# Performance work log

Measured on AMD Instinct MI355X. Metric: run time of the kernel, lower is better.

## Reference

```python
import jax, jax.numpy as jnp
import numpy as np


def _prelu(x, a):
    return jnp.where(x >= 0, x, a * x)


def _conv1x1(x, w, b, a):
    # x: (B,C,H,W), w: (O,C), b: (O,), a: PReLU scalar (shared, torch default)
    y = jnp.einsum('bchw,oc->bohw', x, w) + b[None, :, None, None]
    return _prelu(y, a)


def setup_inputs() -> dict:
    key = jax.random.key(0)
    ks = jax.random.split(key, 7)
    B, C, H, W = 8, 128, 256, 256
    std = 1.0 / np.sqrt(C)
    x = jax.random.normal(ks[0], (B, C, H, W), dtype=jnp.float32)
    Wf = jax.random.normal(ks[1], (C, C), dtype=jnp.float32) * std
    bf = jax.random.normal(ks[2], (C,), dtype=jnp.float32) * std
    Wg = jax.random.normal(ks[3], (C, C), dtype=jnp.float32) * std
    bg = jax.random.normal(ks[4], (C,), dtype=jnp.float32) * std
    Wh = jax.random.normal(ks[5], (C, C), dtype=jnp.float32) * std
    bh = jax.random.normal(ks[6], (C,), dtype=jnp.float32) * std
    af = jnp.float32(0.25)
    ag = jnp.float32(0.25)
    ah = jnp.float32(0.25)
    return {"x": x, "Wf": Wf, "bf": bf, "af": af,
            "Wg": Wg, "bg": bg, "ag": ag,
            "Wh": Wh, "bh": bh, "ah": ah}


def reference(x, Wf, bf, af, Wg, bg, ag, Wh, bh, ah):
    # 1x1 conv projections + PReLU
    map_f = _conv1x1(x, Wf, bf, af)          # (B,C,H,W)
    map_g = _conv1x1(x, Wg, bg, ag)          # (B,C,H,W)
    map_h = _conv1x1(x, Wh, bh, ah)          # (B,C,H,W)
    # map_f.transpose(2,3) @ map_g -> (B,C,W,W), unscaled single-head attention
    atten = jnp.einsum('bchw,bchv->bcwv', map_f, map_g)  # (B,C,W,W)
    atten = jax.nn.softmax(atten, axis=-1)
    # map_h @ atten -> (B,C,H,W)
    out = jnp.einsum('bchw,bcwv->bchv', map_h, atten)
    return out + x
```

## Files before the change

### kernel.cpp

```cpp
#include <hip/hip_runtime.h>

typedef __bf16 bf16_t;
typedef __bf16 bf16x8 __attribute__((ext_vector_type(8)));
typedef __bf16 bf16x4 __attribute__((ext_vector_type(4)));
typedef float  f32x4  __attribute__((ext_vector_type(4)));

#define HW_ 65536
#define C_  128

__device__ __forceinline__ int swz(int r) { return ((r ^ (r >> 3)) & 7) << 4; }

#define LGKM0() asm volatile("s_waitcnt lgkmcnt(0)" ::: "memory")
__device__ __forceinline__ void BAR() {
  asm volatile("" ::: "memory");
  __builtin_amdgcn_s_barrier();
  asm volatile("" ::: "memory");
}

template<bool HBLK>
__device__ __forceinline__ void conv_one(char* lds, const float* __restrict__ Wsrc,
                                         const float* __restrict__ bias, float alpha,
                                         bf16_t* __restrict__ dst, size_t pb,
                                         int wv, int lr, int lq, int t, int s0)
{
  __syncthreads();
  #pragma unroll
  for (int rep = 0; rep < 16; ++rep) {
    int q = rep * 256 + t;
    int o = q >> 5, c0 = (q & 31) * 4;
    f32x4 w4 = *(const f32x4*)(Wsrc + o * C_ + c0);
    bf16x4 v;
    v[0] = (bf16_t)w4[0]; v[1] = (bf16_t)w4[1]; v[2] = (bf16_t)w4[2]; v[3] = (bf16_t)w4[3];
    *(bf16x4*)(lds + 32768 + ((o * 256 + c0 * 2) ^ swz(o))) = v;
  }
  __syncthreads();

  const f32x4 fz = {0.f, 0.f, 0.f, 0.f};
  f32x4 acc[2][8];
  #pragma unroll
  for (int mf = 0; mf < 2; ++mf)
    #pragma unroll
    for (int nf = 0; nf < 8; ++nf)
      acc[mf][nf] = fz;

  #pragma unroll
  for (int ks = 0; ks < 4; ++ks) {
    int kb = ks * 32 + lq * 8;
    bf16x8 a[2], bb[8];
    #pragma unroll
    for (int mf = 0; mf < 2; ++mf) {
      int m = wv * 32 + mf * 16 + lr;
      a[mf] = *(const bf16x8*)(lds + 32768 + ((m * 256 + kb * 2) ^ swz(m)));
    }
    #pragma unroll
    for (int nf = 0; nf < 8; ++nf) {
      int n = nf * 16 + lr;
      bb[nf] = *(const bf16x8*)(lds + ((n * 256 + kb * 2) ^ swz(n)));
    }
    #pragma unroll
    for (int mf = 0; mf < 2; ++mf)
      #pragma unroll
      for (int nf = 0; nf < 8; ++nf)
        acc[mf][nf] = __builtin_amdgcn_mfma_f32_16x16x32_bf16(a[mf], bb[nf], acc[mf][nf], 0, 0, 0);
  }

  #pragma unroll
  for (int mf = 0; mf < 2; ++mf) {
    #pragma unroll
    for (int i = 0; i < 4; ++i) {
      int o = wv * 32 + mf * 16 + lq * 4 + i;
      float bo = bias[o];
      #pragma unroll
      for (int nf = 0; nf < 8; ++nf) {
        int s = s0 + nf * 16 + lr;
        float v = acc[mf][nf][i] + bo;
        v = (v >= 0.f) ? v : alpha * v;
        size_t off;
        if (HBLK) {
          int h = s >> 8, w = s & 255;
          off = pb + (size_t)o * HW_ + (size_t)(w >> 6) * 16384 + h * 64 + (w & 63);
        } else {
          off = pb + (size_t)o * HW_ + s;
        }
        dst[off] = (bf16_t)v;
      }
    }
  }
}

__global__ __launch_bounds__(256, 2) void conv_kernel(
    const float* __restrict__ x,
    const float* __restrict__ Wf, const float* __restrict__ bfp, const float* __restrict__ afp,
    const float* __restrict__ Wg, const float* __restrict__ bgp, const float* __restrict__ agp,
    const float* __restrict__ Wh, const float* __restrict__ bhp, const float* __restrict__ ahp,
    bf16_t* __restrict__ mF, bf16_t* __restrict__ mG, bf16_t* __restrict__ mH, int b0)
{
  __shared__ __align__(16) char lds[65536];
  const int t = threadIdx.x;
  const int bloc = blockIdx.y;
  const int s0 = blockIdx.x * 128;
  const size_t xbase = ((size_t)(b0 + bloc) * C_) * HW_ + s0;

  #pragma unroll
  for (int rep = 0; rep < 4; ++rep) {
    int q = rep * 256 + t;
    int c0 = (q >> 5) * 4, sl0 = (q & 31) * 4;
    f32x4 r[4];
    #pragma unroll
    for (int i = 0; i < 4; ++i)
      r[i] = *(const f32x4*)(x + xbase + (size_t)(c0 + i) * HW_ + sl0);
    #pragma unroll
    for (int js = 0; js < 4; ++js) {
      int s = sl0 + js;
      bf16x4 v;
      v[0] = (bf16_t)r[0][js]; v[1] = (bf16_t)r[1][js];
      v[2] = (bf16_t)r[2][js]; v[3] = (bf16_t)r[3][js];
      *(bf16x4*)(lds + ((s * 256 + c0 * 2) ^ swz(s))) = v;
    }
  }

  const int wv = t >> 6, lane = t & 63, lr = lane & 15, lq = lane >> 4;
  const size_t pb = (size_t)bloc * C_ * HW_;
  conv_one<false>(lds, Wf, bfp, afp[0], mF, pb, wv, lr, lq, t, s0);
  conv_one<false>(lds, Wg, bgp, agp[0], mG, pb, wv, lr, lq, t, s0);
  conv_one<true >(lds, Wh, bhp, ahp[0], mH, pb, wv, lr, lq, t, s0);
}

#define GT_OFF  32768
#define HS_OFF  131072
#define SMAX_OFF 151552
#define SSUM_OFF 153600
#define SMEM_BYTES 155648

__global__ __launch_bounds__(512, 2) void attn_kernel(
    const bf16_t* __restrict__ mF, const bf16_t* __restrict__ mG, const bf16_t* __restrict__ mH,
    const float* __restrict__ x, float* __restrict__ out, int b0)
{
  extern __shared__ __align__(16) char smem[];
  const int t = threadIdx.x;
  const int c = blockIdx.x, bloc = blockIdx.y;
  const int wv = t >> 6, lane = t & 63, lr = lane & 15, lq = lane >> 4;
  const int wr = wv >> 1, wc = wv & 1;
  const size_t plane  = ((size_t)bloc * C_ + c) * HW_;
  const size_t gplane = (((size_t)(b0 + bloc)) * C_ + c) * HW_;

  const f32x4 fz = {0.f, 0.f, 0.f, 0.f};
  f32x4 acc[4][8];
  #pragma unroll
  for (int mf = 0; mf < 4; ++mf)
    #pragma unroll
    for (int nf = 0; nf < 8; ++nf)
      acc[mf][nf] = fz;

  const int hq = t >> 5, wb8 = t & 31;

  bf16x8 pfF[4], pfG[4];
  #pragma unroll
  for (int i = 0; i < 4; ++i) {
    pfF[i] = *(const bf16x8*)(mF + plane + (size_t)(hq * 4 + i) * 256 + wb8 * 8);
    pfG[i] = *(const bf16x8*)(mG + plane + (size_t)(hq * 4 + i) * 256 + wb8 * 8);
  }

  for (int hb = 0; hb < 256; hb += 64) {
    BAR();
    #pragma unroll
    for (int j = 0; j < 8; ++j) {
      int w = wb8 * 8 + j;
      bf16x4 v; v[0] = pfF[0][j]; v[1] = pfF[1][j]; v[2] = pfF[2][j]; v[3] = pfF[3][j];
      *(bf16x4*)(smem + ((w * 128 + hq * 8) ^ swz(w))) = v;
      bf16x4 g; g[0] = pfG[0][j]; g[1] = pfG[1][j]; g[2] = pfG[2][j]; g[3] = pfG[3][j];
      *(bf16x4*)(smem + GT_OFF + ((w * 128 + hq * 8) ^ swz(w))) = g;
    }
    if (hb < 192) {
      #pragma unroll
      for (int i = 0; i < 4; ++i) {
        pfF[i] = *(const bf16x8*)(mF + plane + (size_t)(hb + 64 + hq * 4 + i) * 256 + wb8 * 8);
        pfG[i] = *(const bf16x8*)(mG + plane + (size_t)(hb + 64 + hq * 4 + i) * 256 + wb8 * 8);
      }
    }
    LGKM0(); BAR();
    #pragma unroll
    for (int k0 = 0; k0 < 64; k0 += 32) {
      int kb = k0 + lq * 8;
      bf16x8 a[4], bb[8];
      #pragma unroll
      for (int mf = 0; mf < 4; ++mf) {
        int m = wr * 64 + mf * 16 + lr;
        a[mf] = *(const bf16x8*)(smem + ((m * 128 + kb * 2) ^ swz(m)));
      }
      #pragma unroll
      for (int nf = 0; nf < 8; ++nf) {
        int n = wc * 128 + nf * 16 + lr;
        bb[nf] = *(const bf16x8*)(smem + GT_OFF + ((n * 128 + kb * 2) ^ swz(n)));
      }
      #pragma unroll
      for (int mf = 0; mf < 4; ++mf)
        #pragma unroll
        for (int nf = 0; nf < 8; ++nf)
          acc[mf][nf] = __builtin_amdgcn_mfma_f32_16x16x32_bf16(a[mf], bb[nf], acc[mf][nf], 0, 0, 0);
    }
  }

  float* smax = (float*)(smem + SMAX_OFF);
  float* ssum = (float*)(smem + SSUM_OFF);
  float rowm[4][4];
  #pragma unroll
  for (int mf = 0; mf < 4; ++mf)
    #pragma unroll
    for (int i = 0; i < 4; ++i) {
      float m = acc[mf][0][i];
      #pragma unroll
      for (int nf = 1; nf < 8; ++nf) m = fmaxf(m, acc[mf][nf][i]);
      #pragma unroll
      for (int d = 1; d < 16; d <<= 1) m = fmaxf(m, __shfl_xor(m, d));
      rowm[mf][i] = m;
    }
  if (lr == 0) {
    #pragma unroll
    for (int mf = 0; mf < 4; ++mf)
      #pragma unroll
      for (int i = 0; i < 4; ++i)
        smax[wc * 256 + wr * 64 + mf * 16 + lq * 4 + i] = rowm[mf][i];
  }
  __syncthreads();
  float m2[4][4], rs[4][4];
  #pragma unroll
  for (int mf = 0; mf < 4; ++mf)
    #pragma unroll
    for (int i = 0; i < 4; ++i) {
      int w = wr * 64 + mf * 16 + lq * 4 + i;
      m2[mf][i] = fmaxf(smax[w], smax[256 + w]);
      rs[mf][i] = 0.f;
    }
  #pragma unroll
  for (int mf = 0; mf < 4; ++mf)
    #pragma unroll
    for (int nf = 0; nf < 8; ++nf)
      #pragma unroll
      for (int i = 0; i < 4; ++i) {
        float e = __expf(acc[mf][nf][i] - m2[mf][i]);
        acc[mf][nf][i] = e;
        rs[mf][i] += e;
      }
  #pragma unroll
  for (int mf = 0; mf < 4; ++mf)
    #pragma unroll
    for (int i = 0; i < 4; ++i) {
      float s = rs[mf][i];
      #pragma unroll
      for (int d = 1; d < 16; d <<= 1) s += __shfl_xor(s, d);
      rs[mf][i] = s;
    }
  if (lr == 0) {
    #pragma unroll
    for (int mf = 0; mf < 4; ++mf)
      #pragma unroll
      for (int i = 0; i < 4; ++i)
        ssum[wc * 256 + wr * 64 + mf * 16 + lq * 4 + i] = rs[mf][i];
  }
  __syncthreads();
  #pragma unroll
  for (int mf = 0; mf < 4; ++mf)
    #pragma unroll
    for (int i = 0; i < 4; ++i) {
      int w = wr * 64 + mf * 16 + lq * 4 + i;
      float rinv = 1.f / (ssum[w] + ssum[256 + w]);
      #pragma unroll
      for (int nf = 0; nf < 8; ++nf) {
        int v_ = wc * 128 + nf * 16 + lr;
        *(bf16_t*)(smem + ((v_ * 512 + w * 2) ^ swz(v_))) = (bf16_t)(acc[mf][nf][i] * rinv);
      }
    }

  #pragma unroll
  for (int mf = 0; mf < 4; ++mf)
    #pragma unroll
    for (int nf = 0; nf < 8; ++nf)
      acc[mf][nf] = fz;

  bf16x8 hreg[2];
  {
    const size_t hbase0 = plane;
    #pragma unroll
    for (int rep = 0; rep < 2; ++rep) {
      int u = rep * 512 + t;
      int h = u >> 2, wl0 = (u & 3) * 8;
      hreg[rep] = *(const bf16x8*)(mH + hbase0 + h * 64 + wl0);
    }
  }

  for (int wk = 0; wk < 8; ++wk) {
    LGKM0(); BAR();
    {
      #pragma unroll
      for (int rep = 0; rep < 2; ++rep) {
        int u = rep * 512 + t;
        int h = u >> 2, wl0 = (u & 3) * 8;
        *(bf16x8*)(smem + HS_OFF + h * 80 + wl0 * 2) = hreg[rep];
      }
    }
    if (wk < 7) {
      const size_t hbase = plane + (size_t)((wk + 1) >> 1) * 16384 + (size_t)((wk + 1) & 1) * 32;
      #pragma unroll
      for (int rep = 0; rep < 2; ++rep) {
        int u = rep * 512 + t;
        int h = u >> 2, wl0 = (u & 3) * 8;
        hreg[rep] = *(const bf16x8*)(mH + hbase + h * 64 + wl0);
      }
    }
    LGKM0(); BAR();
    int kb = lq * 8;
    bf16x8 a[4], bb[8];
    #pragma unroll
    for (int mf = 0; mf < 4; ++mf) {
      int m = wr * 64 + mf * 16 + lr;
      a[mf] = *(const bf16x8*)(smem + HS_OFF + m * 80 + kb * 2);
    }
    #pragma unroll
    for (int nf = 0; nf < 8; ++nf) {
      int n = wc * 128 + nf * 16 + lr;
      int kg = wk * 32 + kb;
      bb[nf] = *(const bf16x8*)(smem + ((n * 512 + kg * 2) ^ swz(n)));
    }
    #pragma unroll
    for (int mf = 0; mf < 4; ++mf)
      #pragma unroll
      for (int nf = 0; nf < 8; ++nf)
        acc[mf][nf] = __builtin_amdgcn_mfma_f32_16x16x32_bf16(a[mf], bb[nf], acc[mf][nf], 0, 0, 0);
  }

  #pragma unroll
  for (int mf = 0; mf < 4; ++mf)
    #pragma unroll
    for (int i = 0; i < 4; ++i) {
      int h = wr * 64 + mf * 16 + lq * 4 + i;
      #pragma unroll
      for (int nf = 0; nf < 8; ++nf) {
        int v_ = wc * 128 + nf * 16 + lr;
        size_t off = gplane + (size_t)h * 256 + v_;
        out[off] = acc[mf][nf][i] + x[off];
      }
    }
}

extern "C" void kernel_launch(void* const* d_in, const int* in_sizes, int n_in,
                              void* d_out, int out_size, void* d_ws, size_t ws_size,
                              hipStream_t stream)
{
  (void)in_sizes; (void)n_in; (void)out_size;
  const float* x   = (const float*)d_in[0];
  const float* Wf  = (const float*)d_in[1];
  const float* bfp = (const float*)d_in[2];
  const float* afp = (const float*)d_in[3];
  const float* Wg  = (const float*)d_in[4];
  const float* bgp = (const float*)d_in[5];
  const float* agp = (const float*)d_in[6];
  const float* Wh  = (const float*)d_in[7];
  const float* bhp = (const float*)d_in[8];
  const float* ahp = (const float*)d_in[9];
  float* out = (float*)d_out;

  const size_t per_map_b = (size_t)C_ * HW_ * sizeof(bf16_t);
  int nb = 1;
  if      (ws_size >= 3 * 8 * per_map_b) nb = 8;
  else if (ws_size >= 3 * 4 * per_map_b) nb = 4;
  else if (ws_size >= 3 * 2 * per_map_b) nb = 2;

  hipFuncSetAttribute(reinterpret_cast<const void*>(attn_kernel),
                      hipFuncAttributeMaxDynamicSharedMemorySize, SMEM_BYTES);

  bf16_t* mF = (bf16_t*)d_ws;
  bf16_t* mG = mF + (size_t)nb * C_ * HW_;
  bf16_t* mH = mG + (size_t)nb * C_ * HW_;

  for (int b0 = 0; b0 < 8; b0 += nb) {
    conv_kernel<<<dim3(512, nb), 256, 0, stream>>>(x, Wf, bfp, afp, Wg, bgp, agp,
                                                   Wh, bhp, ahp, mF, mG, mH, b0);
    attn_kernel<<<dim3(C_, nb), 512, SMEM_BYTES, stream>>>(mF, mG, mH, x, out, b0);
  }
}
```

Baseline: 394.7 us.

## Prefetch F/G tiles two stages ahead and stream residual x during PV loop

The F/G staging loop now keeps two register buffers, so global loads for tile ci+2 are issued while tile ci is consumed, and the loop is fully unrolled. The residual x values are loaded in slices during the output GEMM loop and added into the accumulators early, instead of being read in the epilogue. The goal is to hide global-load latency for both the attention inputs and the residual. The cost is more live VGPRs on top of a 128-register accumulator, which risks lower occupancy or spills.

```diff
diff --git a/kernel.cpp b/kernel.cpp
--- a/kernel.cpp
+++ b/kernel.cpp
@@ -154,28 +154,34 @@
 
   const int hq = t >> 5, wb8 = t & 31;
 
-  bf16x8 pfF[4], pfG[4];
-  #pragma unroll
-  for (int i = 0; i < 4; ++i) {
-    pfF[i] = *(const bf16x8*)(mF + plane + (size_t)(hq * 4 + i) * 256 + wb8 * 8);
-    pfG[i] = *(const bf16x8*)(mG + plane + (size_t)(hq * 4 + i) * 256 + wb8 * 8);
-  }
-
-  for (int hb = 0; hb < 256; hb += 64) {
+  bf16x8 pfF[2][4], pfG[2][4];
+  #pragma unroll
+  for (int p = 0; p < 2; ++p)
+    #pragma unroll
+    for (int i = 0; i < 4; ++i) {
+      pfF[p][i] = *(const bf16x8*)(mF + plane + (size_t)(p * 64 + hq * 4 + i) * 256 + wb8 * 8);
+      pfG[p][i] = *(const bf16x8*)(mG + plane + (size_t)(p * 64 + hq * 4 + i) * 256 + wb8 * 8);
+    }
+
+  #pragma unroll
+  for (int ci = 0; ci < 4; ++ci) {
+    const int buf = ci & 1;
     BAR();
     #pragma unroll
     for (int j = 0; j < 8; ++j) {
       int w = wb8 * 8 + j;
-      bf16x4 v; v[0] = pfF[0][j]; v[1] = pfF[1][j]; v[2] = pfF[2][j]; v[3] = pfF[3][j];
+      bf16x4 v; v[0] = pfF[buf][0][j]; v[1] = pfF[buf][1][j];
+      v[2] = pfF[buf][2][j]; v[3] = pfF[buf][3][j];
       *(bf16x4*)(smem + ((w * 128 + hq * 8) ^ swz(w))) = v;
-      bf16x4 g; g[0] = pfG[0][j]; g[1] = pfG[1][j]; g[2] = pfG[2][j]; g[3] = pfG[3][j];
+      bf16x4 g; g[0] = pfG[buf][0][j]; g[1] = pfG[buf][1][j];
+      g[2] = pfG[buf][2][j]; g[3] = pfG[buf][3][j];
       *(bf16x4*)(smem + GT_OFF + ((w * 128 + hq * 8) ^ swz(w))) = g;
     }
-    if (hb < 192) {
+    if (ci < 2) {
       #pragma unroll
       for (int i = 0; i < 4; ++i) {
-        pfF[i] = *(const bf16x8*)(mF + plane + (size_t)(hb + 64 + hq * 4 + i) * 256 + wb8 * 8);
-        pfG[i] = *(const bf16x8*)(mG + plane + (size_t)(hb + 64 + hq * 4 + i) * 256 + wb8 * 8);
+        pfF[buf][i] = *(const bf16x8*)(mF + plane + (size_t)((ci + 2) * 64 + hq * 4 + i) * 256 + wb8 * 8);
+        pfG[buf][i] = *(const bf16x8*)(mG + plane + (size_t)((ci + 2) * 64 + hq * 4 + i) * 256 + wb8 * 8);
       }
     }
     LGKM0(); BAR();
@@ -280,15 +286,22 @@
 
   bf16x8 hreg[2];
   {
-    const size_t hbase0 = plane;
     #pragma unroll
     for (int rep = 0; rep < 2; ++rep) {
       int u = rep * 512 + t;
       int h = u >> 2, wl0 = (u & 3) * 8;
-      hreg[rep] = *(const bf16x8*)(mH + hbase0 + h * 64 + wl0);
-    }
-  }
-
+      hreg[rep] = *(const bf16x8*)(mH + plane + h * 64 + wl0);
+    }
+  }
+  float xv[16];
+  #pragma unroll
+  for (int n0 = 0; n0 < 4; ++n0)
+    #pragma unroll
+    for (int i = 0; i < 4; ++i)
+      xv[n0 * 4 + i] = x[gplane + (size_t)(wr * 64 + lq * 4 + i) * 256
+                         + wc * 128 + n0 * 16 + lr];
+
+  #pragma unroll
   for (int wk = 0; wk < 8; ++wk) {
     LGKM0(); BAR();
     {
@@ -309,7 +322,7 @@
       }
     }
     LGKM0(); BAR();
-    int kb = lq * 8;
+    const int kb = lq * 8;
     bf16x8 a[4], bb[8];
     #pragma unroll
     for (int mf = 0; mf < 4; ++mf) {
@@ -327,6 +340,24 @@
       #pragma unroll
       for (int nf = 0; nf < 8; ++nf)
         acc[mf][nf] = __builtin_amdgcn_mfma_f32_16x16x32_bf16(a[mf], bb[nf], acc[mf][nf], 0, 0, 0);
+
+    {
+      const int mfb = wk >> 1, nhb = wk & 1;
+      #pragma unroll
+      for (int n0 = 0; n0 < 4; ++n0)
+        #pragma unroll
+        for (int i = 0; i < 4; ++i)
+          acc[mfb][nhb * 4 + n0][i] += xv[n0 * 4 + i];
+      if (wk < 7) {
+        const int mfn = (wk + 1) >> 1, nhn = (wk + 1) & 1;
+        #pragma unroll
+        for (int n0 = 0; n0 < 4; ++n0)
+          #pragma unroll
+          for (int i = 0; i < 4; ++i)
+            xv[n0 * 4 + i] = x[gplane + (size_t)(wr * 64 + mfn * 16 + lq * 4 + i) * 256
+                               + wc * 128 + (nhn * 4 + n0) * 16 + lr];
+      }
+    }
   }
 
   #pragma unroll
@@ -337,8 +368,7 @@
       #pragma unroll
       for (int nf = 0; nf < 8; ++nf) {
         int v_ = wc * 128 + nf * 16 + lr;
-        size_t off = gplane + (size_t)h * 256 + v_;
-        out[off] = acc[mf][nf][i] + x[off];
+        out[gplane + (size_t)h * 256 + v_] = acc[mf][nf][i];
       }
     }
 }
```

New measurement: 490.6 us. 24.3% more time.
